# Performance work log

Measured on AMD Instinct MI355X. Metric: run time of the kernel, lower is better.

Reference implementation:

```python
import jax, jax.numpy as jnp
import numpy as np

N = 100   # num_nodes
D = 32    # num_dags
B = 8192  # batch_size
H = 32    # MLP hidden width


def setup_inputs() -> dict:
    key = jax.random.key(0)
    ks = jax.random.split(key, 6)
    x = jax.random.normal(ks[0], (B, N), dtype=jnp.float32)
    # binary adjacency masks for each sampled DAG
    A = (jax.random.uniform(ks[1], (D, N, N)) < 0.5).astype(jnp.float32)
    # per-dag topological order: a permutation of the N nodes
    order = jax.vmap(lambda k: jax.random.permutation(k, N))(
        jax.random.split(ks[2], D)).astype(jnp.int32)
    do_idx = 0  # intervened node
    # per-node MLP params: Linear(N+1, H) -> LeakyReLU -> Linear(H, 1)
    W1 = jax.random.normal(ks[3], (N, H, N + 1), dtype=jnp.float32) * (1.0 / np.sqrt(N + 1))
    b1 = jnp.zeros((N, H), dtype=jnp.float32)
    W2 = jax.random.normal(ks[4], (N, H), dtype=jnp.float32) * (1.0 / np.sqrt(H))
    b2 = jnp.zeros((N,), dtype=jnp.float32)
    return {"x": x, "A": A, "order": order, "do_idx": do_idx,
            "W1": W1, "b1": b1, "W2": W2, "b2": b2}


def reference(x, A, order, do_idx, W1, b1, W2, b2):
    Bn, Nn = x.shape
    # intervention: zero incoming edges of do_idx
    A = A.at[:, :, do_idx].set(0.0)

    def run_dag(A_d, order_d):
        def step(outputs, node):
            mask = A_d[:, node]                      # [N] parents of `node`
            ins = jnp.concatenate(
                [outputs * mask[None, :], x[:, node][:, None]], axis=1)  # [B, N+1]
            h = jax.nn.leaky_relu(ins @ W1[node].T + b1[node])           # [B, H]
            out = h @ W2[node] + b2[node]                                # [B]
            val = jnp.where(node == do_idx, x[:, node], out)
            return outputs.at[:, node].set(val), None

        outs, _ = jax.lax.scan(step, jnp.zeros((Bn, Nn), x.dtype), order_d)
        return outs  # [B, N]

    return jax.vmap(run_dag)(A, order)  # [D, B, N]
```

## Files before the change

kernel.cpp:

```cpp
#include <hip/hip_runtime.h>
#include <hip/hip_fp16.h>

#define NN 100
#define HH 32
#define BB 8192
#define DD 32
#define KP 128
#define TPB 1024

typedef _Float16 f16x8 __attribute__((ext_vector_type(8)));
typedef __fp16 fph2 __attribute__((ext_vector_type(2)));
typedef _Float16 f16x2 __attribute__((ext_vector_type(2)));
typedef float f32x4 __attribute__((ext_vector_type(4)));
typedef unsigned short ushort_t;
typedef unsigned int uint_t;
union FU { uint4 u; f16x8 h; };
union PU { fph2 p; f16x2 h; uint_t u; };

#define AS_GLOBAL __attribute__((address_space(1)))
#define AS_LDS    __attribute__((address_space(3)))

#define SELQ(arr, qq) ((qq) == 0 ? arr[0] : (qq) == 1 ? arr[1] : (qq) == 2 ? arr[2] : arr[3])

#define EPI4_OFF 65536
#define B2T_OFF 71936
#define SMEM_BYTES 72336

__global__ void prep_xth(const float* __restrict__ x, ushort_t* __restrict__ xTh) {
  int idx = blockIdx.x * 256 + threadIdx.x;
  if (idx >= BB * NN) return;
  int b = idx & (BB - 1);
  int n = idx >> 13;
  xTh[idx] = __half_as_ushort(__float2half_rn(x[(size_t)b * NN + n]));
}

__global__ void prep_w1m(const float* __restrict__ A, const float* __restrict__ W1,
                         const float* __restrict__ b1, ushort_t* __restrict__ W1M) {
  int idx = blockIdx.x * 256 + threadIdx.x;
  int tile = idx >> 12;
  int d = tile / NN;
  int node = tile - d * NN;
  int rem = idx & 4095;
  int j = rem >> 7;
  int k = rem & 127;
  float v = 0.f;
  if (k < NN) {
    float m = A[((size_t)d * NN + k) * NN + node];
    v = (m != 0.f) ? W1[((size_t)node * HH + j) * (NN + 1) + k] : 0.f;
  } else if (k == NN) {
    v = W1[((size_t)node * HH + j) * (NN + 1) + NN];
  } else if (k == NN + 1) {
    v = b1[node * HH + j];
  }
  int t = (j * KP + k) ^ ((j & 7) << 3);
  W1M[(size_t)tile * 4096 + t] = __half_as_ushort(__float2half_rn(v));
}

__global__ void prep_epi4(const float* __restrict__ W2, const float* __restrict__ b2,
                          uint_t* __restrict__ epi4, float* __restrict__ b2t) {
  int idx = blockIdx.x * 256 + threadIdx.x;
  if (idx < NN * 16) {
    int node = idx >> 4;
    int g = (idx >> 2) & 3;
    int r = idx & 3;
    int j0 = ((r & 2) << 3) + 4 * g + ((r & 1) << 1);
    uint_t lo = __half_as_ushort(__float2half_rn(W2[node * HH + j0]));
    uint_t hi = __half_as_ushort(__float2half_rn(W2[node * HH + j0 + 1]));
    epi4[idx] = lo | (hi << 16);
  } else if (idx < NN * 16 + NN) {
    int node = idx - NN * 16;
    b2t[node] = b2[node];
  }
}

__global__ __launch_bounds__(TPB, 4) void dag_mfma_w64(
    const ushort_t* __restrict__ xTh,
    const int* __restrict__ order,
    const int* __restrict__ do_idx_p,
    const ushort_t* __restrict__ W1M,
    const uint_t* __restrict__ epi4_g,
    const float* __restrict__ b2t_g,
    float* __restrict__ out)
{
  __shared__ __align__(16) char smem[SMEM_BYTES];
  const char* sp = (const char*)smem;

  const int d = blockIdx.y;
  const int bx = blockIdx.x;
  const int tid = threadIdx.x;
  const int w = tid >> 6;
  const int lane = tid & 63;
  const int g = lane >> 4;
  const int n16 = lane & 15;
  const int di = __builtin_amdgcn_readfirstlane(do_idx_p[0]);
  const int* ord = order + d * NN;
  const int rowbase = bx * 1024 + w * 64 + n16;

  {
    const uint4* s4 = (const uint4*)epi4_g;
    uint4* d4 = (uint4*)(smem + EPI4_OFF);
    for (int i = tid; i < 400; i += TPB) d4[i] = s4[i];
    if (tid < NN) ((float*)(smem + B2T_OFF))[tid] = b2t_g[tid];
  }

  const ushort_t* Wd = W1M + (size_t)d * NN * 4096;

  int vs[4];
#pragma unroll
  for (int S = 0; S < 4; ++S) {
    int hw = n16 * KP + ((8 * g) ^ ((n16 & 3) << 3)) + 32 * (S ^ ((n16 >> 2) & 1));
    vs[S] = 2 * hw;
  }
  int tsb = 32768;

  int nd[4], nn2[4];
#pragma unroll
  for (int q = 0; q < 4; ++q) { nd[q] = __builtin_amdgcn_readfirstlane(ord[q]); nn2[q] = nd[q]; }
  {
    const int q2 = tid >> 8, sub = tid & 255;
    const int nsel = SELQ(nd, q2);
    const char* gb = (const char*)(Wd + (size_t)nsel * 4096);
    char* lb = (char*)smem + q2 * 8192;
    __builtin_amdgcn_global_load_lds((const AS_GLOBAL void*)(gb + sub * 16),
                                     (AS_LDS void*)(lb + sub * 16), 16, 0, 0);
    __builtin_amdgcn_global_load_lds((const AS_GLOBAL void*)(gb + 4096 + sub * 16),
                                     (AS_LDS void*)(lb + 4096 + sub * 16), 16, 0, 0);
  }
  ushort_t xbc[4], xbn[4];
  {
    const ushort_t* xp = xTh + (size_t)nd[0] * BB + rowbase;
#pragma unroll
    for (int nt = 0; nt < 4; ++nt) xbc[nt] = xp[nt * 16];
  }

  uint4 breg[4][4];
#pragma unroll
  for (int nt = 0; nt < 4; ++nt) {
#pragma unroll
    for (int S = 0; S < 4; ++S) breg[nt][S] = make_uint4(0u, 0u, 0u, 0u);
    breg[nt][3].z = (g == 0) ? 0x3C000000u : 0u;
  }

  const f32x4 zero4 = {0.f, 0.f, 0.f, 0.f};
  PU c001; c001.u = 0x211F211Fu;

#pragma unroll 1
  for (int ss = 0; ss < 25; ++ss) {
    asm volatile("s_waitcnt vmcnt(0) lgkmcnt(0)" ::: "memory");
    __builtin_amdgcn_s_barrier();
    __builtin_amdgcn_sched_barrier(0);

    tsb ^= 32768;

    if (ss < 24) {
#pragma unroll
      for (int q = 0; q < 4; ++q)
        nn2[q] = __builtin_amdgcn_readfirstlane(ord[4 * (ss + 1) + q]);
      const int dset = tsb ^ 32768;
      const int q2 = tid >> 8, sub = tid & 255;
      const int nsel = SELQ(nn2, q2);
      const char* gb = (const char*)(Wd + (size_t)nsel * 4096);
      char* lb = (char*)smem + dset + q2 * 8192;
      __builtin_amdgcn_global_load_lds((const AS_GLOBAL void*)(gb + sub * 16),
                                       (AS_LDS void*)(lb + sub * 16), 16, 0, 0);
      __builtin_amdgcn_global_load_lds((const AS_GLOBAL void*)(gb + 4096 + sub * 16),
                                       (AS_LDS void*)(lb + 4096 + sub * 16), 16, 0, 0);
    }

#pragma unroll
    for (int q = 0; q < 4; ++q) {
      const int node = nd[q];

      {
        const int node_nx = (q < 3) ? nd[q + 1] : nn2[0];
        const ushort_t* xp = xTh + (size_t)node_nx * BB + rowbase;
#pragma unroll
        for (int nt = 0; nt < 4; ++nt) xbn[nt] = xp[nt * 16];
      }

#pragma unroll
      for (int nt = 0; nt < 4; ++nt) {
        uint_t ins = 0x3C000000u | (uint_t)xbc[nt];
        breg[nt][3].z = (g == 0) ? ins : breg[nt][3].z;
      }

      float val[4];
      if (node != di) {
        const uint4 w4 = *(const uint4*)(sp + EPI4_OFF + node * 64 + g * 16);
        const float b2n = *(const float*)(sp + B2T_OFF + node * 4);
        const int tb = tsb + q * 8192;

        f32x4 acc[4];
        float p0[4];

        __builtin_amdgcn_s_setprio(1);
#pragma unroll
        for (int S = 0; S < 4; ++S) {
          FU a;
          a.u = *(const uint4*)(sp + tb + vs[S]);
#pragma unroll
          for (int nt = 0; nt < 4; ++nt) {
            FU bu; bu.u = breg[nt][S];
            if (S == 0)
              acc[nt] = __builtin_amdgcn_mfma_f32_16x16x32_f16(a.h, bu.h, zero4, 0, 0, 0);
            else
              acc[nt] = __builtin_amdgcn_mfma_f32_16x16x32_f16(a.h, bu.h, acc[nt], 0, 0, 0);
          }
        }
        __builtin_amdgcn_s_setprio(0);
        {
          PU w01, w23; w01.u = w4.x; w23.u = w4.y;
#pragma unroll
          for (int nt = 0; nt < 4; ++nt) {
            PU h01, h23;
            h01.p = __builtin_amdgcn_cvt_pkrtz(acc[nt][0], acc[nt][1]);
            h23.p = __builtin_amdgcn_cvt_pkrtz(acc[nt][2], acc[nt][3]);
            h01.p = __builtin_elementwise_max(h01.p, h01.p * c001.p);
            h23.p = __builtin_elementwise_max(h23.p, h23.p * c001.p);
            float p = __builtin_amdgcn_fdot2(h01.h, w01.h, 0.f, false);
            p0[nt] = __builtin_amdgcn_fdot2(h23.h, w23.h, p, false);
          }
        }

        __builtin_amdgcn_s_setprio(1);
#pragma unroll
        for (int S = 0; S < 4; ++S) {
          FU a;
          a.u = *(const uint4*)(sp + tb + 4096 + vs[S]);
#pragma unroll
          for (int nt = 0; nt < 4; ++nt) {
            FU bu; bu.u = breg[nt][S];
            if (S == 0)
              acc[nt] = __builtin_amdgcn_mfma_f32_16x16x32_f16(a.h, bu.h, zero4, 0, 0, 0);
            else
              acc[nt] = __builtin_amdgcn_mfma_f32_16x16x32_f16(a.h, bu.h, acc[nt], 0, 0, 0);
          }
        }
        __builtin_amdgcn_s_setprio(0);
        {
          PU w45, w67; w45.u = w4.z; w67.u = w4.w;
#pragma unroll
          for (int nt = 0; nt < 4; ++nt) {
            PU h45, h67;
            h45.p = __builtin_amdgcn_cvt_pkrtz(acc[nt][0], acc[nt][1]);
            h67.p = __builtin_amdgcn_cvt_pkrtz(acc[nt][2], acc[nt][3]);
            h45.p = __builtin_elementwise_max(h45.p, h45.p * c001.p);
            h67.p = __builtin_elementwise_max(h67.p, h67.p * c001.p);
            float p = __builtin_amdgcn_fdot2(h45.h, w45.h, p0[nt], false);
            p = __builtin_amdgcn_fdot2(h67.h, w67.h, p, false);
            p += __shfl_xor(p, 16, 64);
            p += __shfl_xor(p, 32, 64);
            val[nt] = p + b2n;
          }
        }
      } else {
#pragma unroll
        for (int nt = 0; nt < 4; ++nt)
          val[nt] = __half2float(__ushort_as_half(xbc[nt]));
      }

      const int sn = node >> 5;
      const int en2 = (node >> 1) & 3;
      const int gn = (node >> 3) & 3;
      const int hin = node & 1;
      const bool own = (g == gn);
      ushort_t hv[4];
#pragma unroll
      for (int nt = 0; nt < 4; ++nt) hv[nt] = __half_as_ushort(__float2half_rn(val[nt]));
#pragma unroll
      for (int S = 0; S < 4; ++S) {
        if (S != sn) continue;
#pragma unroll
        for (int nt = 0; nt < 4; ++nt) {
          uint4& Bq = breg[nt][S];
          uint_t hvn = (uint_t)hv[nt];
          if (en2 == 0) {
            uint_t old = Bq.x;
            uint_t nw = hin ? ((old & 0x0000FFFFu) | (hvn << 16)) : ((old & 0xFFFF0000u) | hvn);
            Bq.x = own ? nw : old;
          } else if (en2 == 1) {
            uint_t old = Bq.y;
            uint_t nw = hin ? ((old & 0x0000FFFFu) | (hvn << 16)) : ((old & 0xFFFF0000u) | hvn);
            Bq.y = own ? nw : old;
          } else if (en2 == 2) {
            uint_t old = Bq.z;
            uint_t nw = hin ? ((old & 0x0000FFFFu) | (hvn << 16)) : ((old & 0xFFFF0000u) | hvn);
            Bq.z = own ? nw : old;
          } else {
            uint_t old = Bq.w;
            uint_t nw = hin ? ((old & 0x0000FFFFu) | (hvn << 16)) : ((old & 0xFFFF0000u) | hvn);
            Bq.w = own ? nw : old;
          }
        }
      }

#pragma unroll
      for (int nt = 0; nt < 4; ++nt) xbc[nt] = xbn[nt];
    }

#pragma unroll
    for (int q = 0; q < 4; ++q) nd[q] = nn2[q];
  }

  __syncthreads();
  ushort_t* tbuf = (ushort_t*)smem;
#pragma unroll 1
  for (int c = 0; c < 16; ++c) {
    __syncthreads();
    if (w == c) {
#pragma unroll
      for (int nt = 0; nt < 4; ++nt) {
        int r = nt * 16 + n16;
#pragma unroll
        for (int S = 0; S < 4; ++S) {
          int k = 32 * S + 8 * g;
          *(uint2*)&tbuf[r * 132 + k] = make_uint2(breg[nt][S].x, breg[nt][S].y);
          *(uint2*)&tbuf[r * 132 + k + 4] = make_uint2(breg[nt][S].z, breg[nt][S].w);
        }
      }
    }
    __syncthreads();
    const size_t obase = ((size_t)d * BB + bx * 1024 + c * 64) * NN;
    for (int idx = tid; idx < 64 * NN; idx += TPB) {
      int rl = idx / NN;
      int col = idx - rl * NN;
      out[obase + idx] = __half2float(__ushort_as_half(tbuf[rl * 132 + col]));
    }
  }
}

extern "C" void kernel_launch(void* const* d_in, const int* in_sizes, int n_in,
                              void* d_out, int out_size, void* d_ws, size_t ws_size,
                              hipStream_t stream) {
  const float* x     = (const float*)d_in[0];
  const float* A     = (const float*)d_in[1];
  const int* order   = (const int*)d_in[2];
  const int* do_idx  = (const int*)d_in[3];
  const float* W1    = (const float*)d_in[4];
  const float* b1    = (const float*)d_in[5];
  const float* W2    = (const float*)d_in[6];
  const float* b2    = (const float*)d_in[7];
  float* out = (float*)d_out;

  char* ws = (char*)d_ws;
  const size_t XTH_B = (size_t)BB * NN * 2;
  const size_t W1M_B = (size_t)DD * NN * 4096 * 2;
  ushort_t* xTh = (ushort_t*)ws;
  ushort_t* W1M = (ushort_t*)(ws + XTH_B);
  uint_t* epi4  = (uint_t*)(ws + XTH_B + W1M_B);
  float* b2t    = (float*)(ws + XTH_B + W1M_B + 6400);

  hipLaunchKernelGGL(prep_xth, dim3((BB * NN) / 256), dim3(256), 0, stream, x, xTh);
  hipLaunchKernelGGL(prep_w1m, dim3((DD * NN * 4096) / 256), dim3(256), 0, stream,
                     A, W1, b1, W1M);
  hipLaunchKernelGGL(prep_epi4, dim3((NN * 16 + NN + 255) / 256), dim3(256), 0, stream,
                     W2, b2, epi4, b2t);
  hipLaunchKernelGGL(dag_mfma_w64, dim3(BB / 1024, DD), dim3(TPB), 0, stream,
                     xTh, order, do_idx, W1M, epi4, b2t, out);
}
```

Measured before the change: 284.0 us.

## Halve rows per wave, double grid, and compute W2 epilogue with MFMA

Each wave now handles 32 batch rows instead of 64, so the grid doubles to 512 blocks and the launch-bounds occupancy hint rises to 8. The two hidden-half GEMMs are interleaved in one loop, giving independent MFMA chains. The second-layer dot product is done as an extra MFMA against a masked W2 row with the bias folded into the accumulator, replacing the fdot2 and cross-lane shuffle reduction. This spreads the serial per-node chain across more waves to hide latency. In exchange, each W1 tile loaded into LDS is reused across fewer rows, which raises LDS traffic per useful FLOP.

```diff
diff --git a/kernel.cpp b/kernel.cpp
--- a/kernel.cpp
+++ b/kernel.cpp
@@ -73,7 +73,7 @@
   }
 }
 
-__global__ __launch_bounds__(TPB, 4) void dag_mfma_w64(
+__global__ __launch_bounds__(TPB, 8) void dag_mfma_em(
     const ushort_t* __restrict__ xTh,
     const int* __restrict__ order,
     const int* __restrict__ do_idx_p,
@@ -94,7 +94,7 @@
   const int n16 = lane & 15;
   const int di = __builtin_amdgcn_readfirstlane(do_idx_p[0]);
   const int* ord = order + d * NN;
-  const int rowbase = bx * 1024 + w * 64 + n16;
+  const int rowbase = bx * 512 + w * 32 + n16;
 
   {
     const uint4* s4 = (const uint4*)epi4_g;
@@ -126,16 +126,16 @@
     __builtin_amdgcn_global_load_lds((const AS_GLOBAL void*)(gb + 4096 + sub * 16),
                                      (AS_LDS void*)(lb + 4096 + sub * 16), 16, 0, 0);
   }
-  ushort_t xbc[4], xbn[4];
+  ushort_t xbc[2], xbn[2];
   {
     const ushort_t* xp = xTh + (size_t)nd[0] * BB + rowbase;
-#pragma unroll
-    for (int nt = 0; nt < 4; ++nt) xbc[nt] = xp[nt * 16];
-  }
-
-  uint4 breg[4][4];
-#pragma unroll
-  for (int nt = 0; nt < 4; ++nt) {
+    xbc[0] = xp[0];
+    xbc[1] = xp[16];
+  }
+
+  uint4 breg[2][4];
+#pragma unroll
+  for (int nt = 0; nt < 2; ++nt) {
 #pragma unroll
     for (int S = 0; S < 4; ++S) breg[nt][S] = make_uint4(0u, 0u, 0u, 0u);
     breg[nt][3].z = (g == 0) ? 0x3C000000u : 0u;
@@ -174,89 +174,14 @@
       {
         const int node_nx = (q < 3) ? nd[q + 1] : nn2[0];
         const ushort_t* xp = xTh + (size_t)node_nx * BB + rowbase;
-#pragma unroll
-        for (int nt = 0; nt < 4; ++nt) xbn[nt] = xp[nt * 16];
-      }
-
-#pragma unroll
-      for (int nt = 0; nt < 4; ++nt) {
+        xbn[0] = xp[0];
+        xbn[1] = xp[16];
+      }
+
+#pragma unroll
+      for (int nt = 0; nt < 2; ++nt) {
         uint_t ins = 0x3C000000u | (uint_t)xbc[nt];
         breg[nt][3].z = (g == 0) ? ins : breg[nt][3].z;
-      }
-
-      float val[4];
-      if (node != di) {
-        const uint4 w4 = *(const uint4*)(sp + EPI4_OFF + node * 64 + g * 16);
-        const float b2n = *(const float*)(sp + B2T_OFF + node * 4);
-        const int tb = tsb + q * 8192;
-
-        f32x4 acc[4];
-        float p0[4];
-
-        __builtin_amdgcn_s_setprio(1);
-#pragma unroll
-        for (int S = 0; S < 4; ++S) {
-          FU a;
-          a.u = *(const uint4*)(sp + tb + vs[S]);
-#pragma unroll
-          for (int nt = 0; nt < 4; ++nt) {
-            FU bu; bu.u = breg[nt][S];
-            if (S == 0)
-              acc[nt] = __builtin_amdgcn_mfma_f32_16x16x32_f16(a.h, bu.h, zero4, 0, 0, 0);
-            else
-              acc[nt] = __builtin_amdgcn_mfma_f32_16x16x32_f16(a.h, bu.h, acc[nt], 0, 0, 0);
-          }
-        }
-        __builtin_amdgcn_s_setprio(0);
-        {
-          PU w01, w23; w01.u = w4.x; w23.u = w4.y;
-#pragma unroll
-          for (int nt = 0; nt < 4; ++nt) {
-            PU h01, h23;
-            h01.p = __builtin_amdgcn_cvt_pkrtz(acc[nt][0], acc[nt][1]);
-            h23.p = __builtin_amdgcn_cvt_pkrtz(acc[nt][2], acc[nt][3]);
-            h01.p = __builtin_elementwise_max(h01.p, h01.p * c001.p);
-            h23.p = __builtin_elementwise_max(h23.p, h23.p * c001.p);
-            float p = __builtin_amdgcn_fdot2(h01.h, w01.h, 0.f, false);
-            p0[nt] = __builtin_amdgcn_fdot2(h23.h, w23.h, p, false);
-          }
-        }
-
-        __builtin_amdgcn_s_setprio(1);
-#pragma unroll
-        for (int S = 0; S < 4; ++S) {
-          FU a;
-          a.u = *(const uint4*)(sp + tb + 4096 + vs[S]);
-#pragma unroll
-          for (int nt = 0; nt < 4; ++nt) {
-            FU bu; bu.u = breg[nt][S];
-            if (S == 0)
-              acc[nt] = __builtin_amdgcn_mfma_f32_16x16x32_f16(a.h, bu.h, zero4, 0, 0, 0);
-            else
-              acc[nt] = __builtin_amdgcn_mfma_f32_16x16x32_f16(a.h, bu.h, acc[nt], 0, 0, 0);
-          }
-        }
-        __builtin_amdgcn_s_setprio(0);
-        {
-          PU w45, w67; w45.u = w4.z; w67.u = w4.w;
-#pragma unroll
-          for (int nt = 0; nt < 4; ++nt) {
-            PU h45, h67;
-            h45.p = __builtin_amdgcn_cvt_pkrtz(acc[nt][0], acc[nt][1]);
-            h67.p = __builtin_amdgcn_cvt_pkrtz(acc[nt][2], acc[nt][3]);
-            h45.p = __builtin_elementwise_max(h45.p, h45.p * c001.p);
-            h67.p = __builtin_elementwise_max(h67.p, h67.p * c001.p);
-            float p = __builtin_amdgcn_fdot2(h45.h, w45.h, p0[nt], false);
-            p = __builtin_amdgcn_fdot2(h67.h, w67.h, p, false);
-            p += __shfl_xor(p, 16, 64);
-            p += __shfl_xor(p, 32, 64);
-            val[nt] = p + b2n;
-          }
-        }
-      } else {
-#pragma unroll
-        for (int nt = 0; nt < 4; ++nt)
-          val[nt] = __half2float(__ushort_as_half(xbc[nt]));
       }
 
       const int sn = node >> 5;
@@ -264,14 +189,71 @@
       const int gn = (node >> 3) & 3;
       const int hin = node & 1;
       const bool own = (g == gn);
-      ushort_t hv[4];
-#pragma unroll
-      for (int nt = 0; nt < 4; ++nt) hv[nt] = __half_as_ushort(__float2half_rn(val[nt]));
+
+      ushort_t hv[2];
+      if (node != di) {
+        const uint4 w4 = *(const uint4*)(sp + EPI4_OFF + node * 64 + g * 16);
+        const float b2n = *(const float*)(sp + B2T_OFF + node * 4);
+        const int tb = tsb + q * 8192;
+
+        f32x4 acc0[2], acc1[2];
+
+        __builtin_amdgcn_s_setprio(1);
+#pragma unroll
+        for (int S = 0; S < 4; ++S) {
+          FU a0, a1;
+          a0.u = *(const uint4*)(sp + tb + vs[S]);
+          a1.u = *(const uint4*)(sp + tb + 4096 + vs[S]);
+#pragma unroll
+          for (int nt = 0; nt < 2; ++nt) {
+            FU bu; bu.u = breg[nt][S];
+            if (S == 0) {
+              acc0[nt] = __builtin_amdgcn_mfma_f32_16x16x32_f16(a0.h, bu.h, zero4, 0, 0, 0);
+              acc1[nt] = __builtin_amdgcn_mfma_f32_16x16x32_f16(a1.h, bu.h, zero4, 0, 0, 0);
+            } else {
+              acc0[nt] = __builtin_amdgcn_mfma_f32_16x16x32_f16(a0.h, bu.h, acc0[nt], 0, 0, 0);
+              acc1[nt] = __builtin_amdgcn_mfma_f32_16x16x32_f16(a1.h, bu.h, acc1[nt], 0, 0, 0);
+            }
+          }
+        }
+        __builtin_amdgcn_s_setprio(0);
+
+        const int i0 = 4 * gn;
+        const bool arow = (n16 == i0);
+        uint4 aepi;
+        aepi.x = arow ? w4.x : 0u;
+        aepi.y = arow ? w4.y : 0u;
+        aepi.z = arow ? w4.z : 0u;
+        aepi.w = arow ? w4.w : 0u;
+        const f32x4 cb2 = {b2n, b2n, b2n, b2n};
+
+#pragma unroll
+        for (int nt = 0; nt < 2; ++nt) {
+          PU h01, h23, h45, h67;
+          h01.p = __builtin_amdgcn_cvt_pkrtz(acc0[nt][0], acc0[nt][1]);
+          h23.p = __builtin_amdgcn_cvt_pkrtz(acc0[nt][2], acc0[nt][3]);
+          h45.p = __builtin_amdgcn_cvt_pkrtz(acc1[nt][0], acc1[nt][1]);
+          h67.p = __builtin_amdgcn_cvt_pkrtz(acc1[nt][2], acc1[nt][3]);
+          h01.p = __builtin_elementwise_max(h01.p, h01.p * c001.p);
+          h23.p = __builtin_elementwise_max(h23.p, h23.p * c001.p);
+          h45.p = __builtin_elementwise_max(h45.p, h45.p * c001.p);
+          h67.p = __builtin_elementwise_max(h67.p, h67.p * c001.p);
+          FU bm;
+          bm.u = make_uint4(h01.u, h23.u, h45.u, h67.u);
+          f32x4 dv = __builtin_amdgcn_mfma_f32_16x16x32_f16(
+              ((FU*)&aepi)->h, bm.h, cb2, 0, 0, 0);
+          hv[nt] = __half_as_ushort(__float2half_rn(dv[0]));
+        }
+      } else {
+        hv[0] = xbc[0];
+        hv[1] = xbc[1];
+      }
+
 #pragma unroll
       for (int S = 0; S < 4; ++S) {
         if (S != sn) continue;
 #pragma unroll
-        for (int nt = 0; nt < 4; ++nt) {
+        for (int nt = 0; nt < 2; ++nt) {
           uint4& Bq = breg[nt][S];
           uint_t hvn = (uint_t)hv[nt];
           if (en2 == 0) {
@@ -294,22 +276,21 @@
         }
       }
 
-#pragma unroll
-      for (int nt = 0; nt < 4; ++nt) xbc[nt] = xbn[nt];
+      xbc[0] = xbn[0];
+      xbc[1] = xbn[1];
     }
 
 #pragma unroll
     for (int q = 0; q < 4; ++q) nd[q] = nn2[q];
   }
 
-  __syncthreads();
   ushort_t* tbuf = (ushort_t*)smem;
 #pragma unroll 1
   for (int c = 0; c < 16; ++c) {
     __syncthreads();
     if (w == c) {
 #pragma unroll
-      for (int nt = 0; nt < 4; ++nt) {
+      for (int nt = 0; nt < 2; ++nt) {
         int r = nt * 16 + n16;
 #pragma unroll
         for (int S = 0; S < 4; ++S) {
@@ -320,8 +301,8 @@
       }
     }
     __syncthreads();
-    const size_t obase = ((size_t)d * BB + bx * 1024 + c * 64) * NN;
-    for (int idx = tid; idx < 64 * NN; idx += TPB) {
+    const size_t obase = ((size_t)d * BB + bx * 512 + c * 32) * NN;
+    for (int idx = tid; idx < 32 * NN; idx += TPB) {
       int rl = idx / NN;
       int col = idx - rl * NN;
       out[obase + idx] = __half2float(__ushort_as_half(tbuf[rl * 132 + col]));
@@ -355,6 +336,6 @@
                      A, W1, b1, W1M);
   hipLaunchKernelGGL(prep_epi4, dim3((NN * 16 + NN + 255) / 256), dim3(256), 0, stream,
                      W2, b2, epi4, b2t);
-  hipLaunchKernelGGL(dag_mfma_w64, dim3(BB / 1024, DD), dim3(TPB), 0, stream,
+  hipLaunchKernelGGL(dag_mfma_em, dim3(BB / 512, DD), dim3(TPB), 0, stream,
                      xTh, order, do_idx, W1M, epi4, b2t, out);
 }
```

Result: slower. 717.5 us (+152.6%).
